# Optimization experiments

Measured on AMD Instinct MI355X. Metric: run time of the kernel, lower is better.

## Reference

```python
import jax, jax.numpy as jnp
import numpy as np

LEAKY_SLOPE = 0.01  # torch.nn.LeakyReLU default negative_slope

N_NODES = 100000
LATENT = 64
N_EDGES = 3200000
HIDDEN = 32


def setup_inputs() -> dict:
    key = jax.random.key(0)
    k_z, k_e0, k_e1, k_w1, k_b1, k_w2, k_b2 = jax.random.split(key, 7)
    z = jax.random.normal(k_z, (N_NODES, LATENT), dtype=jnp.float32)
    edge_idx = jnp.stack([
        jax.random.randint(k_e0, (N_EDGES,), 0, N_NODES),
        jax.random.randint(k_e1, (N_EDGES,), 0, N_NODES),
    ]).astype(jnp.int64 if jax.config.jax_enable_x64 else jnp.int32)
    in_dim = 2 * LATENT
    # torch Linear default init: U(-1/sqrt(fan_in), 1/sqrt(fan_in))
    s1 = 1.0 / np.sqrt(in_dim)
    s2 = 1.0 / np.sqrt(HIDDEN)
    W1 = jax.random.uniform(k_w1, (in_dim, HIDDEN), minval=-s1, maxval=s1, dtype=jnp.float32)
    b1 = jax.random.uniform(k_b1, (HIDDEN,), minval=-s1, maxval=s1, dtype=jnp.float32)
    W2 = jax.random.uniform(k_w2, (HIDDEN, 1), minval=-s2, maxval=s2, dtype=jnp.float32)
    b2 = jax.random.uniform(k_b2, (1,), minval=-s2, maxval=s2, dtype=jnp.float32)
    return {"z": z, "edge_idx": edge_idx, "W1": W1, "b1": b1, "W2": W2, "b2": b2}


def reference(z, edge_idx, W1, b1, W2, b2):
    # Gather node pairs and concat: [E, 2*latent_dim]
    node_pairs = jnp.concatenate([z[edge_idx[0]], z[edge_idx[1]]], axis=1)
    # Linear -> LeakyReLU (Dropout is identity at inference) -> Linear -> tanh
    h = node_pairs @ W1 + b1                    # [E, hidden]
    h = jnp.where(h >= 0, h, LEAKY_SLOPE * h)   # LeakyReLU
    out = h @ W2 + b2                           # [E, 1]
    return jnp.tanh(out)
```

## Files before the change

### kernel.cpp

```cpp
#include <hip/hip_runtime.h>
#include <hip/hip_fp16.h>
#include <math.h>

#define LEAKY 0.01f

__device__ inline float2 h2f(uint w) {
    __half2 h = *reinterpret_cast<__half2*>(&w);
    return __half22float2(h);
}

__global__ __launch_bounds__(256) void node_proj_uv(
    const float* __restrict__ z, const float* __restrict__ W1,
    const float* __restrict__ b1, __half* __restrict__ U, __half* __restrict__ V,
    int N)
{
    int n = blockIdx.x * blockDim.x + threadIdx.x;
    if (n >= N) return;

    const float4* zr = reinterpret_cast<const float4*>(z + (size_t)n * 64);

    float au[32], av[32];
    #pragma unroll
    for (int j = 0; j < 32; ++j) { au[j] = b1[j]; av[j] = 0.0f; }

    #pragma unroll 4
    for (int k4 = 0; k4 < 16; ++k4) {
        float4 a = zr[k4];
        const float* wu0 = W1 + (4 * k4 + 0) * 32;
        const float* wu1 = W1 + (4 * k4 + 1) * 32;
        const float* wu2 = W1 + (4 * k4 + 2) * 32;
        const float* wu3 = W1 + (4 * k4 + 3) * 32;
        const float* wv0 = wu0 + 64 * 32;
        const float* wv1 = wu1 + 64 * 32;
        const float* wv2 = wu2 + 64 * 32;
        const float* wv3 = wu3 + 64 * 32;
        #pragma unroll
        for (int j = 0; j < 32; ++j) {
            float tu = au[j];
            tu = fmaf(a.x, wu0[j], tu);
            tu = fmaf(a.y, wu1[j], tu);
            tu = fmaf(a.z, wu2[j], tu);
            tu = fmaf(a.w, wu3[j], tu);
            au[j] = tu;
            float tv = av[j];
            tv = fmaf(a.x, wv0[j], tv);
            tv = fmaf(a.y, wv1[j], tv);
            tv = fmaf(a.z, wv2[j], tv);
            tv = fmaf(a.w, wv3[j], tv);
            av[j] = tv;
        }
    }

    uint wu[16], wv[16];
    #pragma unroll
    for (int i = 0; i < 16; ++i) {
        __half2 hu = __floats2half2_rn(au[2 * i], au[2 * i + 1]);
        wu[i] = *reinterpret_cast<uint*>(&hu);
        __half2 hv = __floats2half2_rn(av[2 * i], av[2 * i + 1]);
        wv[i] = *reinterpret_cast<uint*>(&hv);
    }
    uint4* du = reinterpret_cast<uint4*>(U + (size_t)n * 32);
    du[0] = make_uint4(wu[0], wu[1], wu[2], wu[3]);
    du[1] = make_uint4(wu[4], wu[5], wu[6], wu[7]);
    du[2] = make_uint4(wu[8], wu[9], wu[10], wu[11]);
    du[3] = make_uint4(wu[12], wu[13], wu[14], wu[15]);
    uint4* dv = reinterpret_cast<uint4*>(V + (size_t)n * 32);
    dv[0] = make_uint4(wv[0], wv[1], wv[2], wv[3]);
    dv[1] = make_uint4(wv[4], wv[5], wv[6], wv[7]);
    dv[2] = make_uint4(wv[8], wv[9], wv[10], wv[11]);
    dv[3] = make_uint4(wv[12], wv[13], wv[14], wv[15]);
}

__global__ __launch_bounds__(256) void edge_decode_quad(
    const int* __restrict__ idx,
    const __half* __restrict__ U, const __half* __restrict__ V,
    const float* __restrict__ W2, const float* __restrict__ b2,
    float* __restrict__ out, int E)
{
    int t = blockIdx.x * blockDim.x + threadIdx.x;
    int e = t >> 2;
    int p = t & 3;
    if (e >= E) return;
    int s = idx[e];
    int d = idx[E + e];

    uint4 uq = *reinterpret_cast<const uint4*>(U + (size_t)s * 32 + p * 8);
    uint4 vq = *reinterpret_cast<const uint4*>(V + (size_t)d * 32 + p * 8);
    float4 w2a = *reinterpret_cast<const float4*>(W2 + p * 8);
    float4 w2b = *reinterpret_cast<const float4*>(W2 + p * 8 + 4);

    float acc = 0.0f;
    {
        float2 uu, vv; float h0, h1;
        uu = h2f(uq.x); vv = h2f(vq.x);
        h0 = uu.x + vv.x; h1 = uu.y + vv.y;
        h0 = (h0 >= 0.0f) ? h0 : LEAKY * h0;
        h1 = (h1 >= 0.0f) ? h1 : LEAKY * h1;
        acc = fmaf(h0, w2a.x, acc); acc = fmaf(h1, w2a.y, acc);
        uu = h2f(uq.y); vv = h2f(vq.y);
        h0 = uu.x + vv.x; h1 = uu.y + vv.y;
        h0 = (h0 >= 0.0f) ? h0 : LEAKY * h0;
        h1 = (h1 >= 0.0f) ? h1 : LEAKY * h1;
        acc = fmaf(h0, w2a.z, acc); acc = fmaf(h1, w2a.w, acc);
        uu = h2f(uq.z); vv = h2f(vq.z);
        h0 = uu.x + vv.x; h1 = uu.y + vv.y;
        h0 = (h0 >= 0.0f) ? h0 : LEAKY * h0;
        h1 = (h1 >= 0.0f) ? h1 : LEAKY * h1;
        acc = fmaf(h0, w2b.x, acc); acc = fmaf(h1, w2b.y, acc);
        uu = h2f(uq.w); vv = h2f(vq.w);
        h0 = uu.x + vv.x; h1 = uu.y + vv.y;
        h0 = (h0 >= 0.0f) ? h0 : LEAKY * h0;
        h1 = (h1 >= 0.0f) ? h1 : LEAKY * h1;
        acc = fmaf(h0, w2b.z, acc); acc = fmaf(h1, w2b.w, acc);
    }

    acc += __shfl_xor(acc, 1);
    acc += __shfl_xor(acc, 2);

    float r = tanhf(acc + b2[0]);
    if (p == 0) out[e] = r;
}

__global__ __launch_bounds__(256) void edge_mlp_f32(
    const float* __restrict__ z, const int* __restrict__ idx,
    const float* __restrict__ W1, const float* __restrict__ b1,
    const float* __restrict__ W2, const float* __restrict__ b2,
    float* __restrict__ out, int E)
{
    int e = blockIdx.x * blockDim.x + threadIdx.x;
    if (e >= E) return;
    int s = idx[e];
    int d = idx[E + e];
    const float4* zs = reinterpret_cast<const float4*>(z + (size_t)s * 64);
    const float4* zd = reinterpret_cast<const float4*>(z + (size_t)d * 64);

    float h[32];
    #pragma unroll
    for (int j = 0; j < 32; ++j) h[j] = b1[j];

    #pragma unroll 4
    for (int k4 = 0; k4 < 16; ++k4) {
        float4 a = zs[k4];
        float4 b = zd[k4];
        const float* wa0 = W1 + (4 * k4 + 0) * 32;
        const float* wa1 = W1 + (4 * k4 + 1) * 32;
        const float* wa2 = W1 + (4 * k4 + 2) * 32;
        const float* wa3 = W1 + (4 * k4 + 3) * 32;
        const float* wb0 = W1 + (64 + 4 * k4 + 0) * 32;
        const float* wb1 = W1 + (64 + 4 * k4 + 1) * 32;
        const float* wb2 = W1 + (64 + 4 * k4 + 2) * 32;
        const float* wb3 = W1 + (64 + 4 * k4 + 3) * 32;
        #pragma unroll
        for (int j = 0; j < 32; ++j) {
            float acc = h[j];
            acc = fmaf(a.x, wa0[j], acc);
            acc = fmaf(a.y, wa1[j], acc);
            acc = fmaf(a.z, wa2[j], acc);
            acc = fmaf(a.w, wa3[j], acc);
            acc = fmaf(b.x, wb0[j], acc);
            acc = fmaf(b.y, wb1[j], acc);
            acc = fmaf(b.z, wb2[j], acc);
            acc = fmaf(b.w, wb3[j], acc);
            h[j] = acc;
        }
    }

    float acc = b2[0];
    #pragma unroll
    for (int j = 0; j < 32; ++j) {
        float hv = h[j];
        hv = (hv >= 0.0f) ? hv : LEAKY * hv;
        acc = fmaf(hv, W2[j], acc);
    }
    out[e] = tanhf(acc);
}

extern "C" void kernel_launch(void* const* d_in, const int* in_sizes, int n_in,
                              void* d_out, int out_size, void* d_ws, size_t ws_size,
                              hipStream_t stream) {
    const float* z  = (const float*)d_in[0];
    const int*   idx = (const int*)d_in[1];
    const float* W1 = (const float*)d_in[2];
    const float* b1 = (const float*)d_in[3];
    const float* W2 = (const float*)d_in[4];
    const float* b2 = (const float*)d_in[5];
    float* out = (float*)d_out;

    const int E = out_size;
    const int N = in_sizes[0] / 64;

    size_t need = (size_t)2 * N * 32 * sizeof(__half);
    if (ws_size >= need) {
        __half* U = (__half*)d_ws;
        __half* V = U + (size_t)N * 32;
        const int threads = 256;
        node_proj_uv<<<(N + threads - 1) / threads, threads, 0, stream>>>(
            z, W1, b1, U, V, N);
        long long tot = 4LL * E;
        edge_decode_quad<<<(int)((tot + threads - 1) / threads), threads, 0, stream>>>(
            idx, U, V, W2, b2, out, E);
    } else {
        const int threads = 256;
        edge_mlp_f32<<<(E + threads - 1) / threads, threads, 0, stream>>>(
            z, idx, W1, b1, W2, b2, out, E);
    }
}
```

Baseline: 197.5 us.

## Split node projection across 4 threads with LDS weights; decode 4 edges per quad

The node projection now uses four threads per node, each computing 8 of the 32 hidden outputs, with W1 staged in shared memory. This cuts per-thread registers and raises parallelism. The edge decoder makes each quad of threads handle four edges, so each thread issues four independent gathers and the thread count drops to E, which increases memory-level parallelism per thread. It also replaces tanhf with a fast exp/rcp approximation, which risks small accuracy differences.

```diff
diff --git a/kernel.cpp b/kernel.cpp
--- a/kernel.cpp
+++ b/kernel.cpp
@@ -4,121 +4,155 @@
 
 #define LEAKY 0.01f
 
+__device__ inline float fast_tanh(float x) {
+    float e2 = __expf(2.0f * x);
+    return 1.0f - 2.0f * __builtin_amdgcn_rcpf(e2 + 1.0f);
+}
+
 __device__ inline float2 h2f(uint w) {
     __half2 h = *reinterpret_cast<__half2*>(&w);
     return __half22float2(h);
 }
 
-__global__ __launch_bounds__(256) void node_proj_uv(
+__global__ __launch_bounds__(256) void node_proj_g4(
     const float* __restrict__ z, const float* __restrict__ W1,
     const float* __restrict__ b1, __half* __restrict__ U, __half* __restrict__ V,
     int N)
 {
-    int n = blockIdx.x * blockDim.x + threadIdx.x;
+    __shared__ float w1s[128 * 32];
+
+    {
+        const float4* src = reinterpret_cast<const float4*>(W1);
+        float4* dst = reinterpret_cast<float4*>(w1s);
+        int tid = threadIdx.x;
+        #pragma unroll
+        for (int i = 0; i < 4; ++i) dst[tid + 256 * i] = src[tid + 256 * i];
+    }
+    __syncthreads();
+
+    int t = blockIdx.x * blockDim.x + threadIdx.x;
+    int n = t >> 2;
+    int g = t & 3;
     if (n >= N) return;
 
     const float4* zr = reinterpret_cast<const float4*>(z + (size_t)n * 64);
 
-    float au[32], av[32];
-    #pragma unroll
-    for (int j = 0; j < 32; ++j) { au[j] = b1[j]; av[j] = 0.0f; }
+    float au[8], av[8];
+    #pragma unroll
+    for (int j = 0; j < 8; ++j) { au[j] = b1[g * 8 + j]; av[j] = 0.0f; }
 
     #pragma unroll 4
     for (int k4 = 0; k4 < 16; ++k4) {
         float4 a = zr[k4];
-        const float* wu0 = W1 + (4 * k4 + 0) * 32;
-        const float* wu1 = W1 + (4 * k4 + 1) * 32;
-        const float* wu2 = W1 + (4 * k4 + 2) * 32;
-        const float* wu3 = W1 + (4 * k4 + 3) * 32;
-        const float* wv0 = wu0 + 64 * 32;
-        const float* wv1 = wu1 + 64 * 32;
-        const float* wv2 = wu2 + 64 * 32;
-        const float* wv3 = wu3 + 64 * 32;
         #pragma unroll
-        for (int j = 0; j < 32; ++j) {
-            float tu = au[j];
-            tu = fmaf(a.x, wu0[j], tu);
-            tu = fmaf(a.y, wu1[j], tu);
-            tu = fmaf(a.z, wu2[j], tu);
-            tu = fmaf(a.w, wu3[j], tu);
-            au[j] = tu;
-            float tv = av[j];
-            tv = fmaf(a.x, wv0[j], tv);
-            tv = fmaf(a.y, wv1[j], tv);
-            tv = fmaf(a.z, wv2[j], tv);
-            tv = fmaf(a.w, wv3[j], tv);
-            av[j] = tv;
+        for (int c = 0; c < 4; ++c) {
+            int k = 4 * k4 + c;
+            float zk = (c == 0) ? a.x : (c == 1) ? a.y : (c == 2) ? a.z : a.w;
+            const float4* wu = reinterpret_cast<const float4*>(&w1s[k * 32 + g * 8]);
+            const float4* wv = reinterpret_cast<const float4*>(&w1s[(64 + k) * 32 + g * 8]);
+            float4 wu0 = wu[0], wu1 = wu[1];
+            float4 wv0 = wv[0], wv1 = wv[1];
+            au[0] = fmaf(zk, wu0.x, au[0]);
+            au[1] = fmaf(zk, wu0.y, au[1]);
+            au[2] = fmaf(zk, wu0.z, au[2]);
+            au[3] = fmaf(zk, wu0.w, au[3]);
+            au[4] = fmaf(zk, wu1.x, au[4]);
+            au[5] = fmaf(zk, wu1.y, au[5]);
+            au[6] = fmaf(zk, wu1.z, au[6]);
+            au[7] = fmaf(zk, wu1.w, au[7]);
+            av[0] = fmaf(zk, wv0.x, av[0]);
+            av[1] = fmaf(zk, wv0.y, av[1]);
+            av[2] = fmaf(zk, wv0.z, av[2]);
+            av[3] = fmaf(zk, wv0.w, av[3]);
+            av[4] = fmaf(zk, wv1.x, av[4]);
+            av[5] = fmaf(zk, wv1.y, av[5]);
+            av[6] = fmaf(zk, wv1.z, av[6]);
+            av[7] = fmaf(zk, wv1.w, av[7]);
         }
     }
 
-    uint wu[16], wv[16];
-    #pragma unroll
-    for (int i = 0; i < 16; ++i) {
+    uint wu[4], wv[4];
+    #pragma unroll
+    for (int i = 0; i < 4; ++i) {
         __half2 hu = __floats2half2_rn(au[2 * i], au[2 * i + 1]);
         wu[i] = *reinterpret_cast<uint*>(&hu);
         __half2 hv = __floats2half2_rn(av[2 * i], av[2 * i + 1]);
         wv[i] = *reinterpret_cast<uint*>(&hv);
     }
-    uint4* du = reinterpret_cast<uint4*>(U + (size_t)n * 32);
-    du[0] = make_uint4(wu[0], wu[1], wu[2], wu[3]);
-    du[1] = make_uint4(wu[4], wu[5], wu[6], wu[7]);
-    du[2] = make_uint4(wu[8], wu[9], wu[10], wu[11]);
-    du[3] = make_uint4(wu[12], wu[13], wu[14], wu[15]);
-    uint4* dv = reinterpret_cast<uint4*>(V + (size_t)n * 32);
-    dv[0] = make_uint4(wv[0], wv[1], wv[2], wv[3]);
-    dv[1] = make_uint4(wv[4], wv[5], wv[6], wv[7]);
-    dv[2] = make_uint4(wv[8], wv[9], wv[10], wv[11]);
-    dv[3] = make_uint4(wv[12], wv[13], wv[14], wv[15]);
-}
-
-__global__ __launch_bounds__(256) void edge_decode_quad(
+    *reinterpret_cast<uint4*>(U + (size_t)n * 32 + g * 8) = make_uint4(wu[0], wu[1], wu[2], wu[3]);
+    *reinterpret_cast<uint4*>(V + (size_t)n * 32 + g * 8) = make_uint4(wv[0], wv[1], wv[2], wv[3]);
+}
+
+__device__ inline float edge_dot(uint4 uq, uint4 vq, float4 w2a, float4 w2b) {
+    float acc = 0.0f;
+    float2 uu, vv; float h0, h1;
+    uu = h2f(uq.x); vv = h2f(vq.x);
+    h0 = uu.x + vv.x; h1 = uu.y + vv.y;
+    h0 = (h0 >= 0.0f) ? h0 : LEAKY * h0;
+    h1 = (h1 >= 0.0f) ? h1 : LEAKY * h1;
+    acc = fmaf(h0, w2a.x, acc); acc = fmaf(h1, w2a.y, acc);
+    uu = h2f(uq.y); vv = h2f(vq.y);
+    h0 = uu.x + vv.x; h1 = uu.y + vv.y;
+    h0 = (h0 >= 0.0f) ? h0 : LEAKY * h0;
+    h1 = (h1 >= 0.0f) ? h1 : LEAKY * h1;
+    acc = fmaf(h0, w2a.z, acc); acc = fmaf(h1, w2a.w, acc);
+    uu = h2f(uq.z); vv = h2f(vq.z);
+    h0 = uu.x + vv.x; h1 = uu.y + vv.y;
+    h0 = (h0 >= 0.0f) ? h0 : LEAKY * h0;
+    h1 = (h1 >= 0.0f) ? h1 : LEAKY * h1;
+    acc = fmaf(h0, w2b.x, acc); acc = fmaf(h1, w2b.y, acc);
+    uu = h2f(uq.w); vv = h2f(vq.w);
+    h0 = uu.x + vv.x; h1 = uu.y + vv.y;
+    h0 = (h0 >= 0.0f) ? h0 : LEAKY * h0;
+    h1 = (h1 >= 0.0f) ? h1 : LEAKY * h1;
+    acc = fmaf(h0, w2b.z, acc); acc = fmaf(h1, w2b.w, acc);
+    return acc;
+}
+
+__global__ __launch_bounds__(256) void edge_decode_q4(
     const int* __restrict__ idx,
     const __half* __restrict__ U, const __half* __restrict__ V,
     const float* __restrict__ W2, const float* __restrict__ b2,
     float* __restrict__ out, int E)
 {
     int t = blockIdx.x * blockDim.x + threadIdx.x;
-    int e = t >> 2;
     int p = t & 3;
-    if (e >= E) return;
-    int s = idx[e];
-    int d = idx[E + e];
-
-    uint4 uq = *reinterpret_cast<const uint4*>(U + (size_t)s * 32 + p * 8);
-    uint4 vq = *reinterpret_cast<const uint4*>(V + (size_t)d * 32 + p * 8);
+    int e0 = t & ~3;
+    if (e0 >= E) return;
+    int eN = E - 1;
+    int ea = min(e0, eN), eb = min(e0 + 1, eN), ec = min(e0 + 2, eN), ed = min(e0 + 3, eN);
+
+    int s0 = idx[ea], s1 = idx[eb], s2 = idx[ec], s3 = idx[ed];
+    int d0 = idx[E + ea], d1 = idx[E + eb], d2 = idx[E + ec], d3 = idx[E + ed];
+
+    const uint4* Up = reinterpret_cast<const uint4*>(U);
+    const uint4* Vp = reinterpret_cast<const uint4*>(V);
+    uint4 u0 = Up[(size_t)s0 * 4 + p];
+    uint4 u1 = Up[(size_t)s1 * 4 + p];
+    uint4 u2 = Up[(size_t)s2 * 4 + p];
+    uint4 u3 = Up[(size_t)s3 * 4 + p];
+    uint4 v0 = Vp[(size_t)d0 * 4 + p];
+    uint4 v1 = Vp[(size_t)d1 * 4 + p];
+    uint4 v2 = Vp[(size_t)d2 * 4 + p];
+    uint4 v3 = Vp[(size_t)d3 * 4 + p];
+
     float4 w2a = *reinterpret_cast<const float4*>(W2 + p * 8);
     float4 w2b = *reinterpret_cast<const float4*>(W2 + p * 8 + 4);
 
-    float acc = 0.0f;
-    {
-        float2 uu, vv; float h0, h1;
-        uu = h2f(uq.x); vv = h2f(vq.x);
-        h0 = uu.x + vv.x; h1 = uu.y + vv.y;
-        h0 = (h0 >= 0.0f) ? h0 : LEAKY * h0;
-        h1 = (h1 >= 0.0f) ? h1 : LEAKY * h1;
-        acc = fmaf(h0, w2a.x, acc); acc = fmaf(h1, w2a.y, acc);
-        uu = h2f(uq.y); vv = h2f(vq.y);
-        h0 = uu.x + vv.x; h1 = uu.y + vv.y;
-        h0 = (h0 >= 0.0f) ? h0 : LEAKY * h0;
-        h1 = (h1 >= 0.0f) ? h1 : LEAKY * h1;
-        acc = fmaf(h0, w2a.z, acc); acc = fmaf(h1, w2a.w, acc);
-        uu = h2f(uq.z); vv = h2f(vq.z);
-        h0 = uu.x + vv.x; h1 = uu.y + vv.y;
-        h0 = (h0 >= 0.0f) ? h0 : LEAKY * h0;
-        h1 = (h1 >= 0.0f) ? h1 : LEAKY * h1;
-        acc = fmaf(h0, w2b.x, acc); acc = fmaf(h1, w2b.y, acc);
-        uu = h2f(uq.w); vv = h2f(vq.w);
-        h0 = uu.x + vv.x; h1 = uu.y + vv.y;
-        h0 = (h0 >= 0.0f) ? h0 : LEAKY * h0;
-        h1 = (h1 >= 0.0f) ? h1 : LEAKY * h1;
-        acc = fmaf(h0, w2b.z, acc); acc = fmaf(h1, w2b.w, acc);
-    }
-
-    acc += __shfl_xor(acc, 1);
-    acc += __shfl_xor(acc, 2);
-
-    float r = tanhf(acc + b2[0]);
-    if (p == 0) out[e] = r;
+    float a0 = edge_dot(u0, v0, w2a, w2b);
+    float a1 = edge_dot(u1, v1, w2a, w2b);
+    float a2 = edge_dot(u2, v2, w2a, w2b);
+    float a3 = edge_dot(u3, v3, w2a, w2b);
+
+    a0 += __shfl_xor(a0, 1); a0 += __shfl_xor(a0, 2);
+    a1 += __shfl_xor(a1, 1); a1 += __shfl_xor(a1, 2);
+    a2 += __shfl_xor(a2, 1); a2 += __shfl_xor(a2, 2);
+    a3 += __shfl_xor(a3, 1); a3 += __shfl_xor(a3, 2);
+
+    float r = (p == 0) ? a0 : (p == 1) ? a1 : (p == 2) ? a2 : a3;
+    r = fast_tanh(r + b2[0]);
+    int eo = e0 + p;
+    if (eo < E) out[eo] = r;
 }
 
 __global__ __launch_bounds__(256) void edge_mlp_f32(
@@ -194,10 +228,10 @@
         __half* U = (__half*)d_ws;
         __half* V = U + (size_t)N * 32;
         const int threads = 256;
-        node_proj_uv<<<(N + threads - 1) / threads, threads, 0, stream>>>(
+        int nthread_np = 4 * N;
+        node_proj_g4<<<(nthread_np + threads - 1) / threads, threads, 0, stream>>>(
             z, W1, b1, U, V, N);
-        long long tot = 4LL * E;
-        edge_decode_quad<<<(int)((tot + threads - 1) / threads), threads, 0, stream>>>(
+        edge_decode_q4<<<(E + threads - 1) / threads, threads, 0, stream>>>(
             idx, U, V, W2, b2, out, E);
     } else {
         const int threads = 256;
```

New measurement: 183.8 us. 1.07x faster.
